# Kernel tuning notes

Hardware: AMD Instinct MI355X
Metric: run time of the kernel (lower is better)

Reference implementation:

```python
import jax, jax.numpy as jnp
import numpy as np

N = 50000
E = 800000
IN_CH = 128
HID = 64
HEADS = 2
OUT_CH = 5
NEG_SLOPE = 0.2


def glorot(key, shape):
    fan_in, fan_out = shape[0], shape[-1]
    lim = jnp.sqrt(6.0 / (fan_in + fan_out))
    return jax.random.uniform(key, shape, jnp.float32, -lim, lim)


def setup_inputs() -> dict:
    key = jax.random.key(0)
    ks = jax.random.split(key, 20)
    x = jax.random.normal(ks[0], (N, IN_CH), jnp.float32)
    edge_index = jax.random.randint(ks[1], (2, E), 0, N, jnp.int32)
    edge_attr = jax.random.uniform(ks[2], (E, 1), jnp.float32)
    # layer 1: in=128 -> heads=2, out=64 (concat)
    W1l = glorot(ks[3], (IN_CH, HEADS * HID)); b1l = jnp.zeros((HEADS * HID,), jnp.float32)
    W1r = glorot(ks[4], (IN_CH, HEADS * HID)); b1r = jnp.zeros((HEADS * HID,), jnp.float32)
    W1e = glorot(ks[5], (1, HEADS * HID)); b1e = jnp.zeros((HEADS * HID,), jnp.float32)
    att1 = glorot(ks[6], (HEADS, HID))
    bias1 = jnp.zeros((HEADS * HID,), jnp.float32)
    # layer 2: in=128 -> heads=1, out=5
    W2l = glorot(ks[7], (HEADS * HID, OUT_CH)); b2l = jnp.zeros((OUT_CH,), jnp.float32)
    W2r = glorot(ks[8], (HEADS * HID, OUT_CH)); b2r = jnp.zeros((OUT_CH,), jnp.float32)
    W2e = glorot(ks[9], (1, OUT_CH)); b2e = jnp.zeros((OUT_CH,), jnp.float32)
    att2 = glorot(ks[10], (1, OUT_CH))
    bias2 = jnp.zeros((OUT_CH,), jnp.float32)
    return dict(x=x, edge_index=edge_index, edge_attr=edge_attr,
                W1l=W1l, b1l=b1l, W1r=W1r, b1r=b1r, W1e=W1e, b1e=b1e, att1=att1, bias1=bias1,
                W2l=W2l, b2l=b2l, W2r=W2r, b2r=b2r, W2e=W2e, b2e=b2e, att2=att2, bias2=bias2)


def gatv2_layer(x, src, dst, edge_attr, Wl, bl, Wr, br, We, be, att, bias, heads, out_ch, concat):
    n = x.shape[0]
    xl = (x @ Wl + bl).reshape(n, heads, out_ch)   # source transform
    xr = (x @ Wr + br).reshape(n, heads, out_ch)   # target transform
    ee = (edge_attr @ We + be).reshape(-1, heads, out_ch)
    # GATv2 score: a^T LeakyReLU(xl[src] + xr[dst] + e)
    s = xl[src] + xr[dst] + ee                      # [E, H, C]
    s = jnp.where(s > 0, s, NEG_SLOPE * s)
    logits = jnp.einsum('ehc,hc->eh', s, att)       # [E, H]
    # segment softmax over incoming edges of each destination node
    mx = jax.ops.segment_max(logits, dst, num_segments=n)
    ex = jnp.exp(logits - mx[dst])
    den = jax.ops.segment_sum(ex, dst, num_segments=n)
    alpha = ex / den[dst]                           # [E, H]
    msg = alpha[:, :, None] * xl[src]               # [E, H, C]
    out = jax.ops.segment_sum(msg, dst, num_segments=n)  # [N, H, C]
    if concat:
        out = out.reshape(n, heads * out_ch)
    else:
        out = out.mean(axis=1)
    return out + bias


def reference(x, edge_index, edge_attr,
              W1l, b1l, W1r, b1r, W1e, b1e, att1, bias1,
              W2l, b2l, W2r, b2r, W2e, b2e, att2, bias2):
    src, dst = edge_index[0], edge_index[1]
    h = gatv2_layer(x, src, dst, edge_attr, W1l, b1l, W1r, b1r, W1e, b1e, att1, bias1,
                    HEADS, HID, True)
    h = jax.nn.elu(h)
    out = gatv2_layer(h, src, dst, edge_attr, W2l, b2l, W2r, b2r, W2e, b2e, att2, bias2,
                      1, OUT_CH, True)
    return out
```

## Files before the change

kernel.cpp:

```cpp
#include <hip/hip_runtime.h>
#include <hip/hip_bf16.h>
#include <math.h>

#define NN 50000
#define NE 800000
#define CAP 48
#define NEG_SLOPE 0.2f
#define LOG2E 1.44269504088896340736f
#define EPB 4096
#define NPB 196
#define NGB 3125
#define NCB 49
#define CCAP 17408
#define QPB 4

typedef __attribute__((ext_vector_type(8))) short bf16x8;
typedef __attribute__((ext_vector_type(4))) float f32x4;
typedef __attribute__((ext_vector_type(2))) float f32x2;


__device__ __forceinline__ float ldf(const void* p, long i, int isbf) {
    if (isbf) {
        unsigned short raw = ((const unsigned short*)p)[i];
        return __uint_as_float(((unsigned)raw) << 16);
    }
    return ((const float*)p)[i];
}

__device__ __forceinline__ short f2bs(float f) {
    __hip_bfloat16 h = __float2bfloat16(f);
    short s; __builtin_memcpy(&s, &h, 2); return s;
}
__device__ __forceinline__ unsigned short f2bu(float f) {
    __hip_bfloat16 h = __float2bfloat16(f);
    unsigned short s; __builtin_memcpy(&s, &h, 2); return s;
}

__device__ __forceinline__ float red16(float p) {
    p += __int_as_float(__builtin_amdgcn_update_dpp(
             0, __float_as_int(p), 0xB1, 0xF, 0xF, false));
    p += __int_as_float(__builtin_amdgcn_update_dpp(
             0, __float_as_int(p), 0x4E, 0xF, 0xF, false));
    p += __int_as_float(__builtin_amdgcn_update_dpp(
             0, __float_as_int(p), 0x141, 0xF, 0xF, false));
    p += __int_as_float(__builtin_amdgcn_update_dpp(
             0, __float_as_int(p), 0x140, 0xF, 0xF, false));
    return p;
}

__device__ __forceinline__ float red32(float p) {
    p = red16(p);
    p += __int_as_float(__builtin_amdgcn_ds_swizzle(__float_as_int(p), 0x401F));
    return p;
}

__global__ void k_setup_wprep(const void* x, int* flag, unsigned* gcnt,
                              const void* __restrict__ Wl,
                              const void* __restrict__ Wr,
                              unsigned short* __restrict__ bfrag,
                              const void* __restrict__ W1e,
                              const void* __restrict__ att1,
                              const void* __restrict__ bias1,
                              const void* __restrict__ W2l,
                              const void* __restrict__ b2l,
                              const void* __restrict__ W2r,
                              const void* __restrict__ b2r,
                              const void* __restrict__ b2e,
                              const void* __restrict__ W2e,
                              const void* __restrict__ att2,
                              const void* __restrict__ bias2,
                              float* __restrict__ prm) {
    unsigned short raw0 = ((const unsigned short*)x)[(threadIdx.x & 63) * 2];
    float v0 = __uint_as_float(((unsigned)raw0) << 16);
    bool sane = isfinite(v0) && fabsf(v0) > 1e-5f && fabsf(v0) < 1e3f;
    const int isbf = (__popcll(__ballot(sane)) > 32) ? 1 : 0;
    if (blockIdx.x == 128) {
        const int t = threadIdx.x;
        if (t == 0) *flag = isbf;
        if (t >= 192 && t < 192 + NCB) gcnt[t - 192] = 0u;
        if (t < 128) {
            prm[t]       = ldf(W1e, t, isbf);
            prm[128 + t] = ldf(att1, t, isbf) * LOG2E;
            prm[256 + t] = ldf(bias1, t, isbf);
#pragma unroll
            for (int c = 0; c < 5; c++) {
                prm[384 + c * 128 + t]  = ldf(W2l, (long)t * 5 + c, isbf);
                prm[1024 + c * 128 + t] = ldf(W2r, (long)t * 5 + c, isbf);
            }
        } else if (t < 133) {
            const int c = t - 128;
            prm[1664 + c] = ldf(b2l, c, isbf);
            prm[1669 + c] = ldf(b2r, c, isbf) + ldf(b2e, c, isbf);
            prm[1674 + c] = ldf(W2e, c, isbf);
            prm[1679 + c] = ldf(att2, c, isbf) * LOG2E;
            prm[1684 + c] = ldf(bias2, c, isbf);
        }
        return;
    }
    int idx = blockIdx.x * 256 + threadIdx.x;
    int j = idx & 7, lane = (idx >> 3) & 63, ks = (idx >> 9) & 3, nt = idx >> 11;
    int k = ks * 32 + (lane >> 4) * 8 + j;
    int n = nt * 16 + (lane & 15);
    float v = (n < 128) ? ldf(Wl, (long)k * 128 + n, isbf)
                        : ldf(Wr, (long)k * 128 + (n - 128), isbf);
    bfrag[idx] = f2bu(v);
}

__global__ __launch_bounds__(256) void k_part1_lin1(
    const void* __restrict__ x, const unsigned short* __restrict__ bfrag,
    const void* __restrict__ bl, const void* __restrict__ br,
    const void* __restrict__ be1,
    unsigned short* __restrict__ xl, unsigned short* __restrict__ xr,
    const int* __restrict__ ei, const void* __restrict__ ea,
    unsigned* __restrict__ gcnt, uint2* __restrict__ coarse,
    const int* __restrict__ flag) {
    const int isbf = flag[0];
    if (blockIdx.x < NPB) {
        __shared__ unsigned hist[64];
        __shared__ unsigned base[64];
        const int tid = threadIdx.x;
        if (tid < 64) hist[tid] = 0u;
        __syncthreads();
        const long e0 = (long)blockIdx.x * EPB + tid;
        int dv[16];
        unsigned pax[16], lr[16];
#pragma unroll
        for (int k = 0; k < 16; k++) {
            const long e = e0 + k * 256;
            if (e < NE) {
                dv[k] = ei[NE + e];
                pax[k] = (__float_as_uint(ldf(ea, e, isbf)) & 0xffff0000u)
                       | (unsigned)ei[e];
            } else dv[k] = -1;
        }
#pragma unroll
        for (int k = 0; k < 16; k++)
            if (dv[k] >= 0)
                lr[k] = atomicAdd(&hist[dv[k] >> 10], 1u);
        __syncthreads();
        if (tid < 64) {
            const unsigned h = hist[tid];
            base[tid] = h ? atomicAdd(&gcnt[tid], h) : 0u;
        }
        __syncthreads();
#pragma unroll
        for (int k = 0; k < 16; k++) {
            if (dv[k] >= 0) {
                const int cb = dv[k] >> 10;
                const unsigned p = base[cb] + lr[k];
                if (p < CCAP) {
                    uint2 pay;
                    pay.x = pax[k];
                    pay.y = (unsigned)dv[k];
                    coarse[(long)cb * CCAP + p] = pay;
                }
            }
        }
        return;
    }
    const int wave = threadIdx.x >> 6, lane = threadIdx.x & 63;
    const int mrow = lane & 15, quad = lane >> 4;
    const long mbase = (long)(blockIdx.x - NPB) * 16;
    bf16x8 afrag[4];
    if (isbf) {
        const unsigned short* xp = (const unsigned short*)x
                                 + (mbase + mrow) * 128 + quad * 8;
#pragma unroll
        for (int ks = 0; ks < 4; ks++)
            afrag[ks] = *(const bf16x8*)(xp + ks * 32);
    } else {
        const float* xp = (const float*)x + (mbase + mrow) * 128 + quad * 8;
#pragma unroll
        for (int ks = 0; ks < 4; ks++) {
            const float4 u0 = *(const float4*)(xp + ks * 32);
            const float4 u1 = *(const float4*)(xp + ks * 32 + 4);
            bf16x8 a;
            a[0] = f2bs(u0.x); a[1] = f2bs(u0.y); a[2] = f2bs(u0.z); a[3] = f2bs(u0.w);
            a[4] = f2bs(u1.x); a[5] = f2bs(u1.y); a[6] = f2bs(u1.z); a[7] = f2bs(u1.w);
            afrag[ks] = a;
        }
    }
#pragma unroll
    for (int q = 0; q < 4; q++) {
        const int nt = wave * 4 + q;
        f32x4 acc = {0.f, 0.f, 0.f, 0.f};
#pragma unroll
        for (int ks = 0; ks < 4; ks++) {
            const bf16x8 bfr = *(const bf16x8*)(bfrag + ((nt * 4 + ks) * 64 + lane) * 8);
            acc = __builtin_amdgcn_mfma_f32_16x16x32_bf16(afrag[ks], bfr, acc, 0, 0, 0);
        }
        const int ng = nt * 16 + (lane & 15);
        const float bv = (ng < 128)
            ? ldf(bl, ng, isbf)
            : ldf(br, ng - 128, isbf) + ldf(be1, ng - 128, isbf);
        unsigned short* dst = (ng < 128) ? xl : xr;
        const int col = ng & 127;
#pragma unroll
        for (int reg = 0; reg < 4; reg++) {
            const long row = mbase + quad * 4 + reg;
            dst[row * 128 + col] = f2bu(acc[reg] + bv);
        }
    }
}

__global__ __launch_bounds__(256) void k_part2(
    const uint2* __restrict__ coarse, const unsigned* __restrict__ gcnt,
    unsigned* __restrict__ sedge, unsigned* __restrict__ deg) {
    const int cb = blockIdx.x >> 2, q = blockIdx.x & 3;
    const int d0 = cb * 1024 + q * 256;
    __shared__ unsigned lcnt[256];
    const int tid = threadIdx.x;
    lcnt[tid] = 0u;
    __syncthreads();
    const int m = min((int)gcnt[cb], CCAP);
    const uint2* __restrict__ cbp = coarse + (long)cb * CCAP;
    for (int i = tid; i < m; i += 256) {
        const uint2 pay = cbp[i];
        const int ld = (int)pay.y - d0;
        if ((unsigned)ld < 256u) {
            const unsigned pos = atomicAdd(&lcnt[ld], 1u);
            if (pos < CAP)
                sedge[(long)pay.y * CAP + pos] = pay.x;
        }
    }
    __syncthreads();
    const int d = d0 + tid;
    if (d < NN) deg[d] = min(lcnt[tid], (unsigned)CAP);
}

__device__ __forceinline__ void edge1(unsigned eg, const unsigned* __restrict__ xl,
                                      int lane, f32x2 wev, f32x2 xrv, f32x2 atv,
                                      float& lsum, f32x2& accv) {
    const int s = (int)(eg & 0xffffu);
    const float e = __uint_as_float(eg & 0xffff0000u);
    const unsigned* row = xl + ((long)s << 6);
    const unsigned rw = row[lane];
    f32x2 xv;
    xv.x = __uint_as_float(rw << 16);
    xv.y = __uint_as_float(rw & 0xffff0000u);
    f32x2 t = xv + __builtin_elementwise_fma((f32x2){e, e}, wev, xrv);
    t = __builtin_elementwise_max(t, t * (f32x2){NEG_SLOPE, NEG_SLOPE});
    const f32x2 pd = t * atv;
    float p = red32(pd.x + pd.y);
    p = fminf(fmaxf(p, -60.f), 60.f);
    const float w = __builtin_amdgcn_exp2f(p);
    lsum += w;
    accv = __builtin_elementwise_fma((f32x2){w, w}, xv, accv);
}

__global__ __launch_bounds__(256) void k_attn1(
    const unsigned* __restrict__ deg, const unsigned* __restrict__ sedge,
    const unsigned* __restrict__ xl, const unsigned* __restrict__ xr,
    const float* __restrict__ prm,
    unsigned short* __restrict__ xl2b, float* __restrict__ xr2) {
    const int n = __builtin_amdgcn_readfirstlane(
        blockIdx.x * 4 + (threadIdx.x >> 6));
    if (n >= NN) return;
    const int lane = threadIdx.x & 63;
    const unsigned rraw = xr[(long)n * 64 + lane];
    const f32x2 xrv = {__uint_as_float(rraw << 16),
                       __uint_as_float(rraw & 0xffff0000u)};
    const float2 wet = *(const float2*)(prm + 2 * lane);
    const f32x2 wev = {wet.x, wet.y};
    const float2 att_ = *(const float2*)(prm + 128 + 2 * lane);
    const f32x2 atv = {att_.x, att_.y};
    float lsum0 = 0.f, lsum1 = 0.f, lsum2 = 0.f, lsum3 = 0.f;
    f32x2 accv0 = {0.f, 0.f}, accv1 = {0.f, 0.f};
    f32x2 accv2 = {0.f, 0.f}, accv3 = {0.f, 0.f};
    const int dg = (int)__builtin_amdgcn_readfirstlane(deg[n]);
    const long base = (long)n * CAP;
    const uint4* __restrict__ sld = (const uint4*)(sedge + base);
    const int dg4 = dg & ~3;
    int g = 0;
    if (dg4 > 0) {
        uint4 eg4 = sld[0];
        for (g = 0; g < dg4; g += 4) {
            uint4 nxt = eg4;
            if (g + 4 < dg4) nxt = sld[(g >> 2) + 1];
            edge1(eg4.x, xl, lane, wev, xrv, atv, lsum0, accv0);
            edge1(eg4.y, xl, lane, wev, xrv, atv, lsum1, accv1);
            edge1(eg4.z, xl, lane, wev, xrv, atv, lsum2, accv2);
            edge1(eg4.w, xl, lane, wev, xrv, atv, lsum3, accv3);
            eg4 = nxt;
        }
    }
    for (; g < dg; ++g)
        edge1(sedge[base + g], xl, lane, wev, xrv, atv, lsum0, accv0);
    const float l = (lsum0 + lsum1) + (lsum2 + lsum3);
    const f32x2 av = (accv0 + accv1) + (accv2 + accv3);
    const float inv = 1.f / fmaxf(l, 1e-20f);
    const float2 bsv = *(const float2*)(prm + 256 + 2 * lane);
    float h0 = fmaf(av.x, inv, bsv.x);
    float h1 = fmaf(av.y, inv, bsv.y);
    h0 = h0 > 0.f ? h0 : __builtin_amdgcn_exp2f(h0 * LOG2E) - 1.f;
    h1 = h1 > 0.f ? h1 : __builtin_amdgcn_exp2f(h1 * LOG2E) - 1.f;
    float pl[5], pr[5];
#pragma unroll
    for (int c = 0; c < 5; c++) {
        const float2 wl = *(const float2*)(prm + 384 + c * 128 + 2 * lane);
        const float2 wr = *(const float2*)(prm + 1024 + c * 128 + 2 * lane);
        pl[c] = h0 * wl.x + h1 * wl.y;
        pr[c] = h0 * wr.x + h1 * wr.y;
        pl[c] = red16(pl[c]);
        pr[c] = red16(pr[c]);
    }
#pragma unroll
    for (int off = 16; off <= 32; off <<= 1) {
#pragma unroll
        for (int c = 0; c < 5; c++) {
            pl[c] += __shfl_xor(pl[c], off);
            pr[c] += __shfl_xor(pr[c], off);
        }
    }
    if (lane == 0) {
        uint4 pk;
        pk.x = (unsigned)f2bu(pl[0] + prm[1664])
             | ((unsigned)f2bu(pl[1] + prm[1665]) << 16);
        pk.y = (unsigned)f2bu(pl[2] + prm[1666])
             | ((unsigned)f2bu(pl[3] + prm[1667]) << 16);
        pk.z = (unsigned)f2bu(pl[4] + prm[1668]);
        pk.w = 0u;
        *(uint4*)(xl2b + (long)n * 8) = pk;
#pragma unroll
        for (int c = 0; c < 5; c++)
            xr2[(long)n * 8 + c] = pr[c] + prm[1669 + c];
    }
}

__global__ __launch_bounds__(256) void k_attn2(
    const unsigned* __restrict__ deg, const unsigned* __restrict__ sedge,
    const unsigned short* __restrict__ xl2b, const float* __restrict__ xr2,
    const float* __restrict__ prm,
    void* __restrict__ out, const int* __restrict__ flag) {
    const int isbf = flag[0];
    const int n = blockIdx.x * 16 + (threadIdx.x >> 4);
    if (n >= NN) return;
    const int l16 = threadIdx.x & 15;
    f32x4 xrb4; float xrb4s;
    f32x4 wev4; float wev4s;
    f32x4 atv4; float atv4s;
    {
        const float4 r0 = *(const float4*)(xr2 + (long)n * 8);
        xrb4 = (f32x4){r0.x, r0.y, r0.z, r0.w};
        xrb4s = xr2[(long)n * 8 + 4];
        wev4 = (f32x4){prm[1674], prm[1675], prm[1676], prm[1677]};
        wev4s = prm[1678];
        atv4 = (f32x4){prm[1679], prm[1680], prm[1681], prm[1682]};
        atv4s = prm[1683];
    }
    const f32x4 ns4 = {NEG_SLOPE, NEG_SLOPE, NEG_SLOPE, NEG_SLOPE};
    float lw = 0.f, laccs = 0.f;
    f32x4 lacc4 = {0.f, 0.f, 0.f, 0.f};
    const int dg = (int)deg[n];
    const long base = (long)n * CAP;
    for (int idx = l16; idx < dg; idx += 16) {
        const unsigned eg = sedge[base + idx];
        const int s = eg & 0xffffu;
        const float a = __uint_as_float(eg & 0xffff0000u);
        const uint4 u = *(const uint4*)(xl2b + (long)s * 8);
        f32x4 xls4;
        xls4.x = __uint_as_float(u.x << 16);
        xls4.y = __uint_as_float(u.x & 0xffff0000u);
        xls4.z = __uint_as_float(u.y << 16);
        xls4.w = __uint_as_float(u.y & 0xffff0000u);
        const float xlss = __uint_as_float(u.z << 16);
        f32x4 v4 = xls4 + __builtin_elementwise_fma((f32x4){a, a, a, a}, wev4, xrb4);
        v4 = __builtin_elementwise_max(v4, v4 * ns4);
        float vs = xlss + fmaf(a, wev4s, xrb4s);
        vs = fmaxf(vs, NEG_SLOPE * vs);
        const f32x4 pd = v4 * atv4;
        float p = ((pd.x + pd.y) + (pd.z + pd.w)) + vs * atv4s;
        p = fminf(fmaxf(p, -60.f), 60.f);
        const float w = __builtin_amdgcn_exp2f(p);
        lw += w;
        lacc4 = __builtin_elementwise_fma((f32x4){w, w, w, w}, xls4, lacc4);
        laccs = fmaf(w, xlss, laccs);
    }
    lw = red16(lw);
    lacc4.x = red16(lacc4.x);
    lacc4.y = red16(lacc4.y);
    lacc4.z = red16(lacc4.z);
    lacc4.w = red16(lacc4.w);
    laccs = red16(laccs);
    if (l16 == 0) {
        const float inv = 1.f / fmaxf(lw, 1e-20f);
        float o[5] = {lacc4.x, lacc4.y, lacc4.z, lacc4.w, laccs};
#pragma unroll
        for (int c = 0; c < 5; c++) {
            const float v = fmaf(o[c], inv, prm[1684 + c]);
            if (isbf) ((__hip_bfloat16*)out)[(long)n * 5 + c] = __float2bfloat16(v);
            else      ((float*)out)[(long)n * 5 + c] = v;
        }
    }
}

extern "C" void kernel_launch(void* const* d_in, const int* in_sizes, int n_in,
                              void* d_out, int out_size, void* d_ws, size_t ws_size,
                              hipStream_t stream) {
    const void* x    = d_in[0];
    const int*  ei   = (const int*)d_in[1];
    const void* ea   = d_in[2];
    const void* W1l  = d_in[3];
    const void* b1l  = d_in[4];
    const void* W1r  = d_in[5];
    const void* b1r  = d_in[6];
    const void* W1e  = d_in[7];
    const void* b1e  = d_in[8];
    const void* att1 = d_in[9];
    const void* bias1= d_in[10];
    const void* W2l  = d_in[11];
    const void* b2l  = d_in[12];
    const void* W2r  = d_in[13];
    const void* b2r  = d_in[14];
    const void* W2e  = d_in[15];
    const void* b2e  = d_in[16];
    const void* att2 = d_in[17];
    const void* bias2= d_in[18];

    float* W = (float*)d_ws;
    int*            flag    = (int*)W;
    unsigned*       gcnt    = (unsigned*)(W + 100000);
    float*          prm     = W + 110000;
    unsigned*       sedge   = (unsigned*)(W + 120000);
    unsigned*       deg     = (unsigned*)(W + 2520000);
    unsigned short* xl1b    = (unsigned short*)(W + 3400000);
    unsigned short* xr1b    = (unsigned short*)(W + 6600000);
    unsigned short* bfrag   = (unsigned short*)(W + 9800000);
    uint2*          coarse  = (uint2*)(W + 9900000);
    unsigned short* xl2b    = (unsigned short*)(W + 9900000);
    float*          xr2     = W + 10300000;

    k_setup_wprep<<<129, 256, 0, stream>>>(x, flag, gcnt, W1l, W1r, bfrag,
                                           W1e, att1, bias1,
                                           W2l, b2l, W2r, b2r, b2e,
                                           W2e, att2, bias2, prm);
    k_part1_lin1<<<NPB + NGB, 256, 0, stream>>>(
        x, bfrag, b1l, b1r, b1e, xl1b, xr1b, ei, ea, gcnt, coarse, flag);
    k_part2<<<NCB * QPB, 256, 0, stream>>>(coarse, gcnt, sedge, deg);
    k_attn1<<<(NN + 3) / 4, 256, 0, stream>>>(deg, sedge,
                                              (const unsigned*)xl1b, (const unsigned*)xr1b,
                                              prm, xl2b, xr2);
    k_attn2<<<(NN * 16 + 255) / 256, 256, 0, stream>>>(deg, sedge, xl2b, xr2,
                                                       prm, d_out, flag);
}
```

Measured before the change: 215.1 us.

## Regroup preprocessing stages to overlap edge binning with weight prep and GEMM

Moves the coarse edge-binning pass into the setup kernel, where it runs alongside the weight-fragment prep, and merges the fine bucketing (part2) into the GEMM kernel so it runs concurrently with the linear transform. The gcnt reset moves to a hipMemsetAsync so binning can run in the setup launch. This cuts one kernel launch and lets the independent graph preprocessing overlap with the dense work. It adds a memset call, and the part2 blocks now share a launch with the many GEMM blocks.

```diff
diff --git a/kernel.cpp b/kernel.cpp
--- a/kernel.cpp
+++ b/kernel.cpp
@@ -13,6 +13,7 @@
 #define NCB 49
 #define CCAP 17408
 #define QPB 4
+#define NP2 196
 
 typedef __attribute__((ext_vector_type(8))) short bf16x8;
 typedef __attribute__((ext_vector_type(4))) float f32x4;
@@ -34,6 +35,13 @@
 __device__ __forceinline__ unsigned short f2bu(float f) {
     __hip_bfloat16 h = __float2bfloat16(f);
     unsigned short s; __builtin_memcpy(&s, &h, 2); return s;
+}
+
+__device__ __forceinline__ int sniff_bf16(const void* p) {
+    unsigned short raw0 = ((const unsigned short*)p)[(threadIdx.x & 63) * 2];
+    float v0 = __uint_as_float(((unsigned)raw0) << 16);
+    bool sane = isfinite(v0) && fabsf(v0) > 1e-5f && fabsf(v0) < 1e3f;
+    return (__popcll(__ballot(sane)) > 32) ? 1 : 0;
 }
 
 __device__ __forceinline__ float red16(float p) {
@@ -54,30 +62,23 @@
     return p;
 }
 
-__global__ void k_setup_wprep(const void* x, int* flag, unsigned* gcnt,
-                              const void* __restrict__ Wl,
-                              const void* __restrict__ Wr,
-                              unsigned short* __restrict__ bfrag,
-                              const void* __restrict__ W1e,
-                              const void* __restrict__ att1,
-                              const void* __restrict__ bias1,
-                              const void* __restrict__ W2l,
-                              const void* __restrict__ b2l,
-                              const void* __restrict__ W2r,
-                              const void* __restrict__ b2r,
-                              const void* __restrict__ b2e,
-                              const void* __restrict__ W2e,
-                              const void* __restrict__ att2,
-                              const void* __restrict__ bias2,
-                              float* __restrict__ prm) {
-    unsigned short raw0 = ((const unsigned short*)x)[(threadIdx.x & 63) * 2];
-    float v0 = __uint_as_float(((unsigned)raw0) << 16);
-    bool sane = isfinite(v0) && fabsf(v0) > 1e-5f && fabsf(v0) < 1e3f;
-    const int isbf = (__popcll(__ballot(sane)) > 32) ? 1 : 0;
+__global__ __launch_bounds__(256) void k_setup_all(
+    const void* x, int* flag, unsigned* gcnt,
+    const void* __restrict__ Wl, const void* __restrict__ Wr,
+    unsigned short* __restrict__ bfrag,
+    const void* __restrict__ W1e, const void* __restrict__ att1,
+    const void* __restrict__ bias1,
+    const void* __restrict__ W2l, const void* __restrict__ b2l,
+    const void* __restrict__ W2r, const void* __restrict__ b2r,
+    const void* __restrict__ b2e,
+    const void* __restrict__ W2e, const void* __restrict__ att2,
+    const void* __restrict__ bias2, float* __restrict__ prm,
+    const int* __restrict__ ei, const void* __restrict__ ea,
+    uint2* __restrict__ coarse) {
+    const int isbf = sniff_bf16(x);
     if (blockIdx.x == 128) {
         const int t = threadIdx.x;
         if (t == 0) *flag = isbf;
-        if (t >= 192 && t < 192 + NCB) gcnt[t - 192] = 0u;
         if (t < 128) {
             prm[t]       = ldf(W1e, t, isbf);
             prm[128 + t] = ldf(att1, t, isbf) * LOG2E;
@@ -97,70 +98,94 @@
         }
         return;
     }
-    int idx = blockIdx.x * 256 + threadIdx.x;
-    int j = idx & 7, lane = (idx >> 3) & 63, ks = (idx >> 9) & 3, nt = idx >> 11;
-    int k = ks * 32 + (lane >> 4) * 8 + j;
-    int n = nt * 16 + (lane & 15);
-    float v = (n < 128) ? ldf(Wl, (long)k * 128 + n, isbf)
-                        : ldf(Wr, (long)k * 128 + (n - 128), isbf);
-    bfrag[idx] = f2bu(v);
-}
-
-__global__ __launch_bounds__(256) void k_part1_lin1(
+    if (blockIdx.x < 128) {
+        int idx = blockIdx.x * 256 + threadIdx.x;
+        int j = idx & 7, lane = (idx >> 3) & 63, ks = (idx >> 9) & 3, nt = idx >> 11;
+        int k = ks * 32 + (lane >> 4) * 8 + j;
+        int n = nt * 16 + (lane & 15);
+        float v = (n < 128) ? ldf(Wl, (long)k * 128 + n, isbf)
+                            : ldf(Wr, (long)k * 128 + (n - 128), isbf);
+        bfrag[idx] = f2bu(v);
+        return;
+    }
+    __shared__ unsigned hist[64];
+    __shared__ unsigned base[64];
+    const int tid = threadIdx.x;
+    const int pb = blockIdx.x - 129;
+    if (tid < 64) hist[tid] = 0u;
+    __syncthreads();
+    const long e0 = (long)pb * EPB + tid;
+    int dv[16];
+    unsigned pax[16], lr[16];
+#pragma unroll
+    for (int k = 0; k < 16; k++) {
+        const long e = e0 + k * 256;
+        if (e < NE) {
+            dv[k] = ei[NE + e];
+            pax[k] = (__float_as_uint(ldf(ea, e, isbf)) & 0xffff0000u)
+                   | (unsigned)ei[e];
+        } else dv[k] = -1;
+    }
+#pragma unroll
+    for (int k = 0; k < 16; k++)
+        if (dv[k] >= 0)
+            lr[k] = atomicAdd(&hist[dv[k] >> 10], 1u);
+    __syncthreads();
+    if (tid < 64) {
+        const unsigned h = hist[tid];
+        base[tid] = h ? atomicAdd(&gcnt[tid], h) : 0u;
+    }
+    __syncthreads();
+#pragma unroll
+    for (int k = 0; k < 16; k++) {
+        if (dv[k] >= 0) {
+            const int cb = dv[k] >> 10;
+            const unsigned p = base[cb] + lr[k];
+            if (p < CCAP) {
+                uint2 pay;
+                pay.x = pax[k];
+                pay.y = (unsigned)dv[k];
+                coarse[(long)cb * CCAP + p] = pay;
+            }
+        }
+    }
+}
+
+__global__ __launch_bounds__(256) void k_gemm_part2(
     const void* __restrict__ x, const unsigned short* __restrict__ bfrag,
     const void* __restrict__ bl, const void* __restrict__ br,
     const void* __restrict__ be1,
     unsigned short* __restrict__ xl, unsigned short* __restrict__ xr,
-    const int* __restrict__ ei, const void* __restrict__ ea,
-    unsigned* __restrict__ gcnt, uint2* __restrict__ coarse,
+    const uint2* __restrict__ coarse, const unsigned* __restrict__ gcnt,
+    unsigned* __restrict__ sedge, unsigned* __restrict__ deg,
     const int* __restrict__ flag) {
     const int isbf = flag[0];
-    if (blockIdx.x < NPB) {
-        __shared__ unsigned hist[64];
-        __shared__ unsigned base[64];
+    if (blockIdx.x < NP2) {
+        const int cb = blockIdx.x >> 2, q = blockIdx.x & 3;
+        const int d0 = cb * 1024 + q * 256;
+        __shared__ unsigned lcnt[256];
         const int tid = threadIdx.x;
-        if (tid < 64) hist[tid] = 0u;
+        lcnt[tid] = 0u;
         __syncthreads();
-        const long e0 = (long)blockIdx.x * EPB + tid;
-        int dv[16];
-        unsigned pax[16], lr[16];
-#pragma unroll
-        for (int k = 0; k < 16; k++) {
-            const long e = e0 + k * 256;
-            if (e < NE) {
-                dv[k] = ei[NE + e];
-                pax[k] = (__float_as_uint(ldf(ea, e, isbf)) & 0xffff0000u)
-                       | (unsigned)ei[e];
-            } else dv[k] = -1;
-        }
-#pragma unroll
-        for (int k = 0; k < 16; k++)
-            if (dv[k] >= 0)
-                lr[k] = atomicAdd(&hist[dv[k] >> 10], 1u);
+        const int m = min((int)gcnt[cb], CCAP);
+        const uint2* __restrict__ cbp = coarse + (long)cb * CCAP;
+        for (int i = tid; i < m; i += 256) {
+            const uint2 pay = cbp[i];
+            const int ld = (int)pay.y - d0;
+            if ((unsigned)ld < 256u) {
+                const unsigned pos = atomicAdd(&lcnt[ld], 1u);
+                if (pos < CAP)
+                    sedge[(long)pay.y * CAP + pos] = pay.x;
+            }
+        }
         __syncthreads();
-        if (tid < 64) {
-            const unsigned h = hist[tid];
-            base[tid] = h ? atomicAdd(&gcnt[tid], h) : 0u;
-        }
-        __syncthreads();
-#pragma unroll
-        for (int k = 0; k < 16; k++) {
-            if (dv[k] >= 0) {
-                const int cb = dv[k] >> 10;
-                const unsigned p = base[cb] + lr[k];
-                if (p < CCAP) {
-                    uint2 pay;
-                    pay.x = pax[k];
-                    pay.y = (unsigned)dv[k];
-                    coarse[(long)cb * CCAP + p] = pay;
-                }
-            }
-        }
+        const int d = d0 + tid;
+        if (d < NN) deg[d] = min(lcnt[tid], (unsigned)CAP);
         return;
     }
     const int wave = threadIdx.x >> 6, lane = threadIdx.x & 63;
     const int mrow = lane & 15, quad = lane >> 4;
-    const long mbase = (long)(blockIdx.x - NPB) * 16;
+    const long mbase = (long)(blockIdx.x - NP2) * 16;
     bf16x8 afrag[4];
     if (isbf) {
         const unsigned short* xp = (const unsigned short*)x
@@ -201,31 +226,6 @@
             dst[row * 128 + col] = f2bu(acc[reg] + bv);
         }
     }
-}
-
-__global__ __launch_bounds__(256) void k_part2(
-    const uint2* __restrict__ coarse, const unsigned* __restrict__ gcnt,
-    unsigned* __restrict__ sedge, unsigned* __restrict__ deg) {
-    const int cb = blockIdx.x >> 2, q = blockIdx.x & 3;
-    const int d0 = cb * 1024 + q * 256;
-    __shared__ unsigned lcnt[256];
-    const int tid = threadIdx.x;
-    lcnt[tid] = 0u;
-    __syncthreads();
-    const int m = min((int)gcnt[cb], CCAP);
-    const uint2* __restrict__ cbp = coarse + (long)cb * CCAP;
-    for (int i = tid; i < m; i += 256) {
-        const uint2 pay = cbp[i];
-        const int ld = (int)pay.y - d0;
-        if ((unsigned)ld < 256u) {
-            const unsigned pos = atomicAdd(&lcnt[ld], 1u);
-            if (pos < CAP)
-                sedge[(long)pay.y * CAP + pos] = pay.x;
-        }
-    }
-    __syncthreads();
-    const int d = d0 + tid;
-    if (d < NN) deg[d] = min(lcnt[tid], (unsigned)CAP);
 }
 
 __device__ __forceinline__ void edge1(unsigned eg, const unsigned* __restrict__ xl,
@@ -430,13 +430,14 @@
     unsigned short* xl2b    = (unsigned short*)(W + 9900000);
     float*          xr2     = W + 10300000;
 
-    k_setup_wprep<<<129, 256, 0, stream>>>(x, flag, gcnt, W1l, W1r, bfrag,
-                                           W1e, att1, bias1,
-                                           W2l, b2l, W2r, b2r, b2e,
-                                           W2e, att2, bias2, prm);
-    k_part1_lin1<<<NPB + NGB, 256, 0, stream>>>(
-        x, bfrag, b1l, b1r, b1e, xl1b, xr1b, ei, ea, gcnt, coarse, flag);
-    k_part2<<<NCB * QPB, 256, 0, stream>>>(coarse, gcnt, sedge, deg);
+    hipMemsetAsync(gcnt, 0, NCB * sizeof(unsigned), stream);
+    k_setup_all<<<129 + NPB, 256, 0, stream>>>(x, flag, gcnt, W1l, W1r, bfrag,
+                                               W1e, att1, bias1,
+                                               W2l, b2l, W2r, b2r, b2e,
+                                               W2e, att2, bias2, prm,
+                                               ei, ea, coarse);
+    k_gemm_part2<<<NP2 + NGB, 256, 0, stream>>>(
+        x, bfrag, b1l, b1r, b1e, xl1b, xr1b, coarse, gcnt, sedge, deg, flag);
     k_attn1<<<(NN + 3) / 4, 256, 0, stream>>>(deg, sedge,
                                               (const unsigned*)xl1b, (const unsigned*)xr1b,
                                               prm, xl2b, xr2);
```

Result: no change. 217.9 us (+1.3%).

## Process two edges per wavefront pass with half-wave channel splitting in attn1

Applied to the files above, without the earlier changes.

Layer-1 attention now splits each 64-lane wavefront into two 32-lane halves, each handling a different edge with 4 channels per lane. The per-edge head reduction needs only red16 instead of red32 and its cross-half swizzle, and each pass covers two edges. The halves' partial sums are merged with a shuffle, then rearranged back to the two-channels-per-lane layout with ds_bpermute. This cuts reduction and exp work per edge, at the cost of extra tail handling and the final permutes.

```diff
diff --git a/kernel.cpp b/kernel.cpp
--- a/kernel.cpp
+++ b/kernel.cpp
@@ -48,10 +48,8 @@
     return p;
 }
 
-__device__ __forceinline__ float red32(float p) {
-    p = red16(p);
-    p += __int_as_float(__builtin_amdgcn_ds_swizzle(__float_as_int(p), 0x401F));
-    return p;
+__device__ __forceinline__ float bperm(int addr4, float v) {
+    return __int_as_float(__builtin_amdgcn_ds_bpermute(addr4, __float_as_int(v)));
 }
 
 __global__ void k_setup_wprep(const void* x, int* flag, unsigned* gcnt,
@@ -228,24 +226,37 @@
     if (d < NN) deg[d] = min(lcnt[tid], (unsigned)CAP);
 }
 
-__device__ __forceinline__ void edge1(unsigned eg, const unsigned* __restrict__ xl,
-                                      int lane, f32x2 wev, f32x2 xrv, f32x2 atv,
-                                      float& lsum, f32x2& accv) {
-    const int s = (int)(eg & 0xffffu);
-    const float e = __uint_as_float(eg & 0xffff0000u);
-    const unsigned* row = xl + ((long)s << 6);
-    const unsigned rw = row[lane];
-    f32x2 xv;
-    xv.x = __uint_as_float(rw << 16);
-    xv.y = __uint_as_float(rw & 0xffff0000u);
-    f32x2 t = xv + __builtin_elementwise_fma((f32x2){e, e}, wev, xrv);
-    t = __builtin_elementwise_max(t, t * (f32x2){NEG_SLOPE, NEG_SLOPE});
-    const f32x2 pd = t * atv;
-    float p = red32(pd.x + pd.y);
+__device__ __forceinline__ void pass2e(unsigned ga, unsigned gb,
+                                       const unsigned* __restrict__ xl,
+                                       int wofs, bool hi,
+                                       const float* we4, const float* xr4,
+                                       const float* at4,
+                                       float& lsum, float* acc) {
+    const int sA = (int)(ga & 0xffffu);
+    const int sB = (int)(gb & 0xffffu);
+    const float eA = __uint_as_float(ga & 0xffff0000u);
+    const float eB = __uint_as_float(gb & 0xffff0000u);
+    const int s = hi ? sB : sA;
+    const float ee = hi ? eB : eA;
+    const uint2 u = *(const uint2*)(xl + ((long)s << 6) + wofs);
+    float xv[4];
+    xv[0] = __uint_as_float(u.x << 16);
+    xv[1] = __uint_as_float(u.x & 0xffff0000u);
+    xv[2] = __uint_as_float(u.y << 16);
+    xv[3] = __uint_as_float(u.y & 0xffff0000u);
+    float pacc = 0.f;
+#pragma unroll
+    for (int j = 0; j < 4; j++) {
+        float t = fmaf(ee, we4[j], xr4[j]) + xv[j];
+        t = fmaxf(t, t * NEG_SLOPE);
+        pacc = fmaf(t, at4[j], pacc);
+    }
+    float p = red16(pacc);
     p = fminf(fmaxf(p, -60.f), 60.f);
     const float w = __builtin_amdgcn_exp2f(p);
     lsum += w;
-    accv = __builtin_elementwise_fma((f32x2){w, w}, xv, accv);
+#pragma unroll
+    for (int j = 0; j < 4; j++) acc[j] = fmaf(w, xv[j], acc[j]);
 }
 
 __global__ __launch_bounds__(256) void k_attn1(
@@ -257,16 +268,25 @@
         blockIdx.x * 4 + (threadIdx.x >> 6));
     if (n >= NN) return;
     const int lane = threadIdx.x & 63;
-    const unsigned rraw = xr[(long)n * 64 + lane];
-    const f32x2 xrv = {__uint_as_float(rraw << 16),
-                       __uint_as_float(rraw & 0xffff0000u)};
-    const float2 wet = *(const float2*)(prm + 2 * lane);
-    const f32x2 wev = {wet.x, wet.y};
-    const float2 att_ = *(const float2*)(prm + 128 + 2 * lane);
-    const f32x2 atv = {att_.x, att_.y};
-    float lsum0 = 0.f, lsum1 = 0.f, lsum2 = 0.f, lsum3 = 0.f;
-    f32x2 accv0 = {0.f, 0.f}, accv1 = {0.f, 0.f};
-    f32x2 accv2 = {0.f, 0.f}, accv3 = {0.f, 0.f};
+    const int hl = lane & 31;
+    const bool hi = lane >= 32;
+    const int cL = ((hl >> 4) << 6) | ((hl & 15) << 2);
+    const int wofs = cL >> 1;
+    const uint2 xru = *(const uint2*)(xr + (long)n * 64 + wofs);
+    float xr4[4], we4[4], at4[4];
+    xr4[0] = __uint_as_float(xru.x << 16);
+    xr4[1] = __uint_as_float(xru.x & 0xffff0000u);
+    xr4[2] = __uint_as_float(xru.y << 16);
+    xr4[3] = __uint_as_float(xru.y & 0xffff0000u);
+    {
+        const float4 wef = *(const float4*)(prm + cL);
+        const float4 atf = *(const float4*)(prm + 128 + cL);
+        we4[0] = wef.x; we4[1] = wef.y; we4[2] = wef.z; we4[3] = wef.w;
+        at4[0] = atf.x; at4[1] = atf.y; at4[2] = atf.z; at4[3] = atf.w;
+    }
+    float lsumA = 0.f, lsumB = 0.f;
+    float accA[4] = {0.f, 0.f, 0.f, 0.f};
+    float accB[4] = {0.f, 0.f, 0.f, 0.f};
     const int dg = (int)__builtin_amdgcn_readfirstlane(deg[n]);
     const long base = (long)n * CAP;
     const uint4* __restrict__ sld = (const uint4*)(sedge + base);
@@ -277,21 +297,60 @@
         for (g = 0; g < dg4; g += 4) {
             uint4 nxt = eg4;
             if (g + 4 < dg4) nxt = sld[(g >> 2) + 1];
-            edge1(eg4.x, xl, lane, wev, xrv, atv, lsum0, accv0);
-            edge1(eg4.y, xl, lane, wev, xrv, atv, lsum1, accv1);
-            edge1(eg4.z, xl, lane, wev, xrv, atv, lsum2, accv2);
-            edge1(eg4.w, xl, lane, wev, xrv, atv, lsum3, accv3);
+            pass2e(eg4.x, eg4.y, xl, wofs, hi, we4, xr4, at4, lsumA, accA);
+            pass2e(eg4.z, eg4.w, xl, wofs, hi, we4, xr4, at4, lsumB, accB);
             eg4 = nxt;
         }
     }
-    for (; g < dg; ++g)
-        edge1(sedge[base + g], xl, lane, wev, xrv, atv, lsum0, accv0);
-    const float l = (lsum0 + lsum1) + (lsum2 + lsum3);
-    const f32x2 av = (accv0 + accv1) + (accv2 + accv3);
-    const float inv = 1.f / fmaxf(l, 1e-20f);
+    if (g + 1 < dg) {
+        pass2e(sedge[base + g], sedge[base + g + 1],
+               xl, wofs, hi, we4, xr4, at4, lsumA, accA);
+        g += 2;
+    }
+    if (g < dg) {
+        const unsigned ga = sedge[base + g];
+        const int s0 = (int)(ga & 0xffffu);
+        const float e0 = __uint_as_float(ga & 0xffff0000u);
+        const uint2 u = *(const uint2*)(xl + ((long)s0 << 6) + wofs);
+        float xv[4];
+        xv[0] = __uint_as_float(u.x << 16);
+        xv[1] = __uint_as_float(u.x & 0xffff0000u);
+        xv[2] = __uint_as_float(u.y << 16);
+        xv[3] = __uint_as_float(u.y & 0xffff0000u);
+        float pacc = 0.f;
+#pragma unroll
+        for (int j = 0; j < 4; j++) {
+            float t = fmaf(e0, we4[j], xr4[j]) + xv[j];
+            t = fmaxf(t, t * NEG_SLOPE);
+            pacc = fmaf(t, at4[j], pacc);
+        }
+        float p = red16(pacc);
+        p = fminf(fmaxf(p, -60.f), 60.f);
+        float w = __builtin_amdgcn_exp2f(p);
+        w = hi ? 0.f : w;
+        lsumA += w;
+#pragma unroll
+        for (int j = 0; j < 4; j++) accA[j] = fmaf(w, xv[j], accA[j]);
+    }
+    float lsum = lsumA + lsumB;
+    float acc[4];
+#pragma unroll
+    for (int j = 0; j < 4; j++) acc[j] = accA[j] + accB[j];
+    lsum += __shfl_xor(lsum, 32);
+#pragma unroll
+    for (int j = 0; j < 4; j++) acc[j] += __shfl_xor(acc[j], 32);
+    const int ls = ((lane >> 5) << 4) + ((lane & 31) >> 1);
+    const int a4 = ls << 2;
+    const float b0 = bperm(a4, acc[0]), b1 = bperm(a4, acc[1]);
+    const float b2 = bperm(a4, acc[2]), b3 = bperm(a4, acc[3]);
+    const float lsr = bperm(a4, lsum);
+    const bool odd = (lane & 1) != 0;
+    const float av0 = odd ? b2 : b0;
+    const float av1 = odd ? b3 : b1;
+    const float inv = 1.f / fmaxf(lsr, 1e-20f);
     const float2 bsv = *(const float2*)(prm + 256 + 2 * lane);
-    float h0 = fmaf(av.x, inv, bsv.x);
-    float h1 = fmaf(av.y, inv, bsv.y);
+    float h0 = fmaf(av0, inv, bsv.x);
+    float h1 = fmaf(av1, inv, bsv.y);
     h0 = h0 > 0.f ? h0 : __builtin_amdgcn_exp2f(h0 * LOG2E) - 1.f;
     h1 = h1 > 0.f ? h1 : __builtin_amdgcn_exp2f(h1 * LOG2E) - 1.f;
     float pl[5], pr[5];
```

After: 212.5 us. About the same (-1.2%).
